# Performance work log

Measured on AMD Instinct MI355X. Metric: run time of the kernel, lower is better.

The kernel has to match this reference:

```python
import jax, jax.numpy as jnp
import numpy as np
from jax import lax

B, N, HID = 2, 2048, 2048
H, KVH, D = 16, 4, 128           # heads, kv heads, head_dim
GROUPS = H // KVH
FLA_WEIGHT = 0.01
NEG = -1e30


def setup_inputs() -> dict:
    key = jax.random.key(0)
    ks = jax.random.split(key, 5)
    s = 0.02
    return {
        "hidden_states": jax.random.normal(ks[0], (B, N, HID), jnp.float32),
        "Wq": jax.random.normal(ks[1], (HID, H * D), jnp.float32) * s,
        "Wk": jax.random.normal(ks[2], (HID, KVH * D), jnp.float32) * s,
        "Wv": jax.random.normal(ks[3], (HID, KVH * D), jnp.float32) * s,
        "Wo": jax.random.normal(ks[4], (H * D, HID), jnp.float32) * s,
    }


def _split_heads(x, h):
    b, n, _ = x.shape
    return x.reshape(b, n, h, -1).transpose(0, 2, 1, 3)  # b h n d


def _gla_attention(q, k, v, scale):
    # Gated linear attention: S_t = sigmoid(k_t) (.) S_{t-1} + k_t (x) v_t,
    # o_t = scale * q_t . S_t ; sequential recurrence over the seq dim.
    qs = jnp.moveaxis(q, 2, 0)  # n b h d
    ks = jnp.moveaxis(k, 2, 0)
    vs = jnp.moveaxis(v, 2, 0)

    def step(S, inp):
        qt, kt, vt = inp                                   # each (b,h,d)
        g = jax.nn.sigmoid(kt)                             # per-key-dim gate
        S = S * g[..., None] + kt[..., None] * vt[..., None, :]  # (b,h,d,dv)
        ot = scale * jnp.einsum('bhd,bhde->bhe', qt, S)
        return S, ot

    S0 = jnp.zeros(q.shape[:2] + (q.shape[-1], v.shape[-1]), q.dtype)
    _, o = lax.scan(step, S0, (qs, ks, vs))                # n b h dv
    return jnp.moveaxis(o, 0, 2)                           # b h n dv


def reference(hidden_states, Wq, Wk, Wv, Wo):
    scale = 1.0 / np.sqrt(D)
    q = _split_heads(hidden_states @ Wq, H)                # b h n d
    k = _split_heads(hidden_states @ Wk, KVH)
    v = _split_heads(hidden_states @ Wv, KVH)
    k = jnp.repeat(k, GROUPS, axis=1)                      # repeat_kv -> b H n d
    v = jnp.repeat(v, GROUPS, axis=1)

    # FLA branch
    fla = _gla_attention(q, k, v, scale)                   # b h n d
    fla = fla.transpose(0, 2, 1, 3).reshape(B, N, H * D)   # b n (h d)

    # Base causal softmax attention
    scores = jnp.einsum('bhnd,bhmd->bhnm', q, k) * scale
    causal = jnp.tril(jnp.ones((N, N), bool))
    scores = jnp.where(causal, scores, NEG)
    attn = jax.nn.softmax(scores, axis=-1)
    base = jnp.einsum('bhnm,bhmd->bhnd', attn, v)
    base = base.transpose(0, 2, 1, 3).reshape(B, N, H * D) @ Wo

    return base + FLA_WEIGHT * fla
```

## Files before the change

### kernel.cpp

```cpp
#include <hip/hip_runtime.h>
#include <hip/hip_bf16.h>
#include <cstdint>
#include <cstddef>


typedef __attribute__((ext_vector_type(4))) float f32x4;
typedef __attribute__((ext_vector_type(2))) float f32x2;
typedef __attribute__((ext_vector_type(8))) short s16x8;
typedef unsigned short u16;
typedef unsigned int u32;

__device__ __forceinline__ float bfu2f(u16 u) {
  union { unsigned int i; float f; } x; x.i = ((unsigned int)u) << 16; return x.f;
}
__device__ __forceinline__ u16 f2bfu(float f) {
  union { float f; unsigned int i; } x; x.f = f;
  unsigned int r = x.i + 0x7fffu + ((x.i >> 16) & 1u);
  return (u16)(r >> 16);
}
__device__ __forceinline__ void bf8_to_f(s16x8 v, float* o) {
  union { s16x8 v; u16 u[8]; } x; x.v = v;
#pragma unroll
  for (int j = 0; j < 8; j++) o[j] = bfu2f(x.u[j]);
}
__device__ __forceinline__ s16x8 pack_bf8(f32x4 lo, f32x4 hi) {
  union { s16x8 v; u16 u[8]; } x;
#pragma unroll
  for (int j = 0; j < 4; j++) { x.u[j] = f2bfu(lo[j]); x.u[4 + j] = f2bfu(hi[j]); }
  return x.v;
}
__device__ __forceinline__ void gload_lds16(const u16* g, u16* l) {
  __builtin_amdgcn_global_load_lds(
      (__attribute__((address_space(1))) void*)(g),
      (__attribute__((address_space(3))) void*)(l), 16, 0, 0);
}

__global__ __launch_bounds__(256) void f32_to_bf16(
    const float* __restrict__ src, u16* __restrict__ dst, int n8) {
  const int i = blockIdx.x * 256 + threadIdx.x;
  if (i < n8) {
    f32x4 a = *(const f32x4*)(src + (size_t)i * 8);
    f32x4 b = *(const f32x4*)(src + (size_t)i * 8 + 4);
    *(s16x8*)(dst + (size_t)i * 8) = pack_bf8(a, b);
  }
}

__global__ __launch_bounds__(256) void transpose_f32_bf16(
    const float* __restrict__ src, u16* __restrict__ dst, int R, int C) {
  __shared__ u16 tile[32][33];
  const int bx = blockIdx.x * 32, by = blockIdx.y * 32;
  const int tx = threadIdx.x & 31, ty = threadIdx.x >> 5;
#pragma unroll
  for (int i = 0; i < 32; i += 8)
    tile[ty + i][tx] = f2bfu(src[(size_t)(by + ty + i) * C + bx + tx]);
  __syncthreads();
#pragma unroll
  for (int i = 0; i < 32; i += 8)
    dst[(size_t)(bx + ty + i) * R + by + tx] = tile[tx][ty + i];
}

__global__ __launch_bounds__(256) void transpose_bf16(
    const u16* __restrict__ src, u16* __restrict__ dst, int R, int C) {
  __shared__ u16 tile[32][33];
  const int bx = blockIdx.x * 32, by = blockIdx.y * 32;
  const int tx = threadIdx.x & 31, ty = threadIdx.x >> 5;
#pragma unroll
  for (int i = 0; i < 32; i += 8)
    tile[ty + i][tx] = src[(size_t)(by + ty + i) * C + bx + tx];
  __syncthreads();
#pragma unroll
  for (int i = 0; i < 32; i += 8)
    dst[(size_t)(bx + ty + i) * R + by + tx] = tile[tx][ty + i];
}

__global__ __launch_bounds__(256) void gemm_qkv(
    const u16* __restrict__ A, const u16* __restrict__ WqT, const u16* __restrict__ WkT,
    const u16* __restrict__ WvT, u16* __restrict__ Qo, u16* __restrict__ Ko,
    u16* __restrict__ Vo) {
  __shared__ u16 Al[128 * 32];
  __shared__ u16 Bl[128 * 32];
  const int bx = blockIdx.x;
  const u16* Bt; u16* Cb; int n0, Nst;
  if (bx < 16)      { Bt = WqT; Cb = Qo; n0 = bx * 128;        Nst = 2048; }
  else if (bx < 20) { Bt = WkT; Cb = Ko; n0 = (bx - 16) * 128; Nst = 512; }
  else              { Bt = WvT; Cb = Vo; n0 = (bx - 20) * 128; Nst = 512; }
  const int K = 2048;
  const int m0 = blockIdx.y * 128;
  const int t = threadIdx.x, w = t >> 6, l = t & 63, lm = l & 15, lq = l >> 4;
  const int wr = w >> 1, wc = w & 1;
  const f32x4 z4 = {0.f, 0.f, 0.f, 0.f};
  f32x4 acc[4][4];
#pragma unroll
  for (int i = 0; i < 4; i++)
#pragma unroll
    for (int j = 0; j < 4; j++) acc[i][j] = z4;
  const int srow = l >> 2, scol = (l & 3) * 8;
  const u16* Ag = A + (size_t)(m0 + w * 32 + srow) * K + scol;
  const u16* Bg = Bt + (size_t)(n0 + w * 32 + srow) * K + scol;
  u16* Alw = &Al[(w * 32) * 32];
  u16* Blw = &Bl[(w * 32) * 32];
  for (int kk = 0; kk < K; kk += 32) {
    gload_lds16(Ag + kk, Alw);
    gload_lds16(Ag + (size_t)16 * K + kk, Alw + 16 * 32);
    gload_lds16(Bg + kk, Blw);
    gload_lds16(Bg + (size_t)16 * K + kk, Blw + 16 * 32);
    __syncthreads();
    s16x8 af[4], bfr[4];
#pragma unroll
    for (int sm = 0; sm < 4; sm++) af[sm] = *(const s16x8*)&Al[(wr * 64 + sm * 16 + lm) * 32 + lq * 8];
#pragma unroll
    for (int sn = 0; sn < 4; sn++) bfr[sn] = *(const s16x8*)&Bl[(wc * 64 + sn * 16 + lm) * 32 + lq * 8];
#pragma unroll
    for (int sm = 0; sm < 4; sm++)
#pragma unroll
      for (int sn = 0; sn < 4; sn++)
        acc[sm][sn] = __builtin_amdgcn_mfma_f32_16x16x32_bf16(af[sm], bfr[sn], acc[sm][sn], 0, 0, 0);
    __syncthreads();
  }
#pragma unroll
  for (int sm = 0; sm < 4; sm++)
#pragma unroll
    for (int sn = 0; sn < 4; sn++)
#pragma unroll
      for (int r = 0; r < 4; r++) {
        const int row = m0 + wr * 64 + sm * 16 + lq * 4 + r;
        const int col = n0 + wc * 64 + sn * 16 + lm;
        Cb[(size_t)row * Nst + col] = f2bfu(acc[sm][sn][r]);
      }
}

__global__ __launch_bounds__(512) void gemm_out2(
    const u16* __restrict__ A, const u16* __restrict__ Bt, float* __restrict__ Cf,
    const u16* __restrict__ addsrc) {
  __shared__ u16 Abuf[3 * 16384];
  __shared__ u16 Bbuf[3 * 8192];
  int f = blockIdx.y * 16 + blockIdx.x;
  f = (f & 7) * 32 + (f >> 3);
  const int by = f >> 4, bx = f & 15;
  const int m0 = by * 256, n0 = bx * 128;
  const int K = 2048, Nst = 2048;
  const int t = threadIdx.x, w = t >> 6, l = t & 63, lm = l & 15, lq = l >> 4;
  const int wr = w >> 1, wc = w & 1;
  const int tr = t >> 3, tc8 = (t & 7) * 8;
  const f32x4 z4 = {0.f, 0.f, 0.f, 0.f};
  f32x4 acc[4][4];
#pragma unroll
  for (int i = 0; i < 4; i++)
#pragma unroll
    for (int j = 0; j < 4; j++) acc[i][j] = z4;
  const u16* Ag = A + (size_t)m0 * K;
  const u16* Bg = Bt + (size_t)n0 * K;
  auto stage = [&](int kt, int bufi) {
#pragma unroll
    for (int i = 0; i < 4; i++) {
      const int row = i * 64 + tr;
      const int col = tc8 ^ ((row & 7) << 3);
      gload_lds16(Ag + (size_t)row * K + kt * 64 + col,
                  Abuf + bufi * 16384 + i * 4096 + w * 512);
    }
#pragma unroll
    for (int i = 0; i < 2; i++) {
      const int row = i * 64 + tr;
      const int col = tc8 ^ ((row & 7) << 3);
      gload_lds16(Bg + (size_t)row * K + kt * 64 + col,
                  Bbuf + bufi * 8192 + i * 4096 + w * 512);
    }
  };
  const int nt = K >> 6;
  stage(0, 0);
  stage(1, 1);
  int cur = 0;
#pragma unroll 1
  for (int kt = 0; kt < nt; kt++) {
    if (kt + 2 < nt) {
      int nb = cur + 2; if (nb >= 3) nb -= 3;
      stage(kt + 2, nb);
      asm volatile("s_waitcnt vmcnt(12)" ::: "memory");
    } else if (kt + 1 < nt) {
      asm volatile("s_waitcnt vmcnt(6)" ::: "memory");
    } else {
      asm volatile("s_waitcnt vmcnt(0)" ::: "memory");
    }
    __builtin_amdgcn_s_barrier();
    const u16* Ab = Abuf + cur * 16384;
    const u16* Bb = Bbuf + cur * 8192;
    s16x8 af[4][2], bff[4][2];
#pragma unroll
    for (int sm = 0; sm < 4; sm++) {
      const int row = wr * 64 + sm * 16 + lm;
#pragma unroll
      for (int kk = 0; kk < 2; kk++)
        af[sm][kk] = *(const s16x8*)&Ab[row * 64 +
            ((((kk << 6) | (lq << 4)) ^ ((row & 7) << 4)) >> 1)];
    }
#pragma unroll
    for (int sn = 0; sn < 4; sn++) {
      const int row = wc * 64 + sn * 16 + lm;
#pragma unroll
      for (int kk = 0; kk < 2; kk++)
        bff[sn][kk] = *(const s16x8*)&Bb[row * 64 +
            ((((kk << 6) | (lq << 4)) ^ ((row & 7) << 4)) >> 1)];
    }
#pragma unroll
    for (int kk = 0; kk < 2; kk++)
#pragma unroll
      for (int sm = 0; sm < 4; sm++)
#pragma unroll
        for (int sn = 0; sn < 4; sn++)
          acc[sm][sn] = __builtin_amdgcn_mfma_f32_16x16x32_bf16(
              af[sm][kk], bff[sn][kk], acc[sm][sn], 0, 0, 0);
    asm volatile("s_waitcnt lgkmcnt(0)" ::: "memory");
    __builtin_amdgcn_s_barrier();
    cur = (cur == 2) ? 0 : cur + 1;
  }
#pragma unroll
  for (int sm = 0; sm < 4; sm++)
#pragma unroll
    for (int sn = 0; sn < 4; sn++)
#pragma unroll
      for (int r = 0; r < 4; r++) {
        const int row = m0 + wr * 64 + sm * 16 + lq * 4 + r;
        const int col = n0 + wc * 64 + sn * 16 + lm;
        float v = acc[sm][sn][r] + 0.01f * bfu2f(addsrc[(size_t)row * Nst + col]);
        Cf[(size_t)row * Nst + col] = v;
      }
}

__global__ __launch_bounds__(512) void flash_attn_wave(
    const u16* __restrict__ Q, const u16* __restrict__ Kx,
    const u16* __restrict__ Vt, u16* __restrict__ AO) {
  __shared__ u16 Klds[2][64 * 128];
  __shared__ u16 Vlds[2][128 * 64];
  __shared__ u16 Pl[8][16][68];
  const int bid = blockIdx.x;
  const int set = bid & 7;
  const int b = set >> 2, kvh = set & 3;
  const int rest = bid >> 3;
  const int j0 = rest >> 1, hp = rest & 1;
  const int t = threadIdx.x, w = t >> 6, l = t & 63, lm = l & 15, lq = l >> 4;
  const int h = kvh * 4 + hp * 2 + (w & 1);
  const int cs = (w >> 1) & 1, mh = w >> 2;
  const float scale2 = 0.127517827f;
  const u16* Kbase = Kx + (size_t)(b * 2048) * 512 + kvh * 128;
  const u16* Vbase = Vt + (size_t)(b * 512 + kvh * 128) * 2048;
  const f32x4 z4 = {0.f, 0.f, 0.f, 0.f};

  auto stage = [&](int kt, int bufi) {
    const int key0 = kt * 64;
#pragma unroll
    for (int r = 0; r < 2; r++) {
      const int row = r * 32 + w * 4 + (l >> 4);
      const int scb = ((l & 15) * 16) ^ ((row & 7) << 4);
      gload_lds16(Kbase + (size_t)(key0 + row) * 512 + (scb >> 1),
                  &Klds[bufi][r * 4096 + w * 512]);
    }
#pragma unroll
    for (int r = 0; r < 2; r++) {
      const int row = r * 64 + w * 8 + (l >> 3);
      const int scb = ((l & 7) * 16) ^ ((row & 7) << 4);
      gload_lds16(Vbase + (size_t)row * 2048 + key0 + (scb >> 1),
                  &Vlds[bufi][r * 4096 + w * 512]);
    }
  };

#pragma unroll 1
  for (int ph = 0; ph < 2; ph++) {
    const int j = ph ? (31 - j0) : j0;
    const int c = 2 * j + cs;
    const int base = c * 32;
    int cur = 0;
    stage(0, 0);
    s16x8 qf[4];
#pragma unroll
    for (int kk = 0; kk < 4; kk++)
      qf[kk] = *(const s16x8*)(Q + ((size_t)(b * 2048 + base + mh * 16 + lm)) * 2048 +
                               h * 128 + kk * 32 + lq * 8);
    f32x4 oacc[8];
#pragma unroll
    for (int e = 0; e < 8; e++) oacc[e] = z4;
    float lsum[4] = {0.f, 0.f, 0.f, 0.f};
#pragma unroll 1
    for (int kt = 0; kt <= j; kt++) {
      const int key0 = kt * 64;
      if (kt < j) {
        stage(kt + 1, cur ^ 1);
        asm volatile("s_waitcnt vmcnt(4)" ::: "memory");
      } else {
        asm volatile("s_waitcnt vmcnt(0)" ::: "memory");
      }
      __builtin_amdgcn_s_barrier();
      const char* KB = (const char*)&Klds[cur][0];
      const char* VB = (const char*)&Vlds[cur][0];
      s16x8 kf[4][4];
#pragma unroll
      for (int nst = 0; nst < 4; nst++)
#pragma unroll
        for (int kk = 0; kk < 4; kk++) {
          const int row = nst * 16 + lm;
          const int cb = (kk * 64 + lq * 16) ^ ((row & 7) << 4);
          kf[nst][kk] = *(const s16x8*)(KB + row * 256 + cb);
        }
      f32x4 sacc[4];
#pragma unroll
      for (int i = 0; i < 4; i++) sacc[i] = z4;
#pragma unroll
      for (int nst = 0; nst < 4; nst++)
#pragma unroll
        for (int kk = 0; kk < 4; kk++)
          sacc[nst] = __builtin_amdgcn_mfma_f32_16x16x32_bf16(
              qf[kk], kf[nst][kk], sacc[nst], 0, 0, 0);
      const bool diag = (kt == j);
#pragma unroll
      for (int r = 0; r < 4; r++) {
        const int qrow = base + mh * 16 + lq * 4 + r;
#pragma unroll
        for (int nst = 0; nst < 4; nst++) {
          float pv = __builtin_amdgcn_exp2f(sacc[nst][r] * scale2);
          if (diag && (key0 + nst * 16 + lm > qrow)) pv = 0.f;
          lsum[r] += pv;
          Pl[w][lq * 4 + r][nst * 16 + lm] = f2bfu(pv);
        }
      }
      s16x8 vf[8][2];
#pragma unroll
      for (int et = 0; et < 8; et++)
#pragma unroll
        for (int kc = 0; kc < 2; kc++) {
          const int row = et * 16 + lm;
          const int cb = (kc * 64 + lq * 16) ^ ((row & 7) << 4);
          vf[et][kc] = *(const s16x8*)(VB + row * 128 + cb);
        }
      s16x8 pf[2];
#pragma unroll
      for (int kc = 0; kc < 2; kc++)
        pf[kc] = *(const s16x8*)&Pl[w][lm][kc * 32 + lq * 8];
#pragma unroll
      for (int et = 0; et < 8; et++)
#pragma unroll
        for (int kc = 0; kc < 2; kc++)
          oacc[et] = __builtin_amdgcn_mfma_f32_16x16x32_bf16(
              pf[kc], vf[et][kc], oacc[et], 0, 0, 0);
      asm volatile("s_waitcnt lgkmcnt(0)" ::: "memory");
      __builtin_amdgcn_s_barrier();
      cur ^= 1;
    }
#pragma unroll
    for (int r = 0; r < 4; r++) {
#pragma unroll
      for (int off = 1; off < 16; off <<= 1)
        lsum[r] += __shfl_xor(lsum[r], off, 64);
    }
#pragma unroll
    for (int r = 0; r < 4; r++) {
      const float inv = 1.f / lsum[r];
      const int row = base + mh * 16 + lq * 4 + r;
      u16* op = AO + ((size_t)(b * 2048 + row)) * 2048 + h * 128;
#pragma unroll
      for (int et = 0; et < 8; et++) op[et * 16 + lm] = f2bfu(oacc[et][r] * inv);
    }
  }
}

__global__ __launch_bounds__(256) void fla_contrib32(
    const u16* __restrict__ Kx, const u16* __restrict__ Vt,
    u16* __restrict__ Gg, u16* __restrict__ Ktg, u16* __restrict__ MT,
    float* __restrict__ Lam) {
  __shared__ float gl[32][132];
  __shared__ float kl[32][132];
  __shared__ float ktl[32][132];
  __shared__ u16 khT[128][40];
  const int c = blockIdx.x, kvh = blockIdx.y, b = blockIdx.z;
  const int bk = b * 4 + kvh;
  const int t = threadIdx.x;
  const size_t cb = (size_t)bk * 64 + c;
  {
    const int r = t >> 3, c0 = (t & 7) * 16;
    const u16* kp = Kx + ((size_t)(b * 2048 + c * 32 + r)) * 512 + kvh * 128 + c0;
#pragma unroll
    for (int i = 0; i < 2; i++) {
      float kv[8];
      bf8_to_f(*(const s16x8*)(kp + i * 8), kv);
#pragma unroll
      for (int j = 0; j < 8; j++) {
        kl[r][c0 + i * 8 + j] = kv[j];
        gl[r][c0 + i * 8 + j] = 1.f / (1.f + __expf(-kv[j]));
      }
    }
  }
  __syncthreads();
  if (t < 128) {
    float G = 1.f;
#pragma unroll
    for (int s = 0; s < 32; s++) {
      G *= gl[s][t];
      gl[s][t] = G;
      ktl[s][t] = kl[s][t] / G;
    }
    Lam[cb * 128 + t] = G;
    const float lam = G;
#pragma unroll
    for (int s = 0; s < 32; s++) khT[t][s] = f2bfu(ktl[s][t] * lam);
  }
  __syncthreads();
  {
    const int r = t >> 3, c0 = (t & 7) * 16;
    u16* gp = Gg + cb * 4096 + r * 128 + c0;
    u16* kp = Ktg + cb * 4096 + r * 128 + c0;
#pragma unroll
    for (int i = 0; i < 2; i++) {
      f32x4 a = *(f32x4*)&gl[r][c0 + i * 8];
      f32x4 b2 = *(f32x4*)&gl[r][c0 + i * 8 + 4];
      *(s16x8*)(gp + i * 8) = pack_bf8(a, b2);
      a = *(f32x4*)&ktl[r][c0 + i * 8];
      b2 = *(f32x4*)&ktl[r][c0 + i * 8 + 4];
      *(s16x8*)(kp + i * 8) = pack_bf8(a, b2);
    }
  }
  const int w = t >> 6, l = t & 63, lm = l & 15, lq = l >> 4;
  const f32x4 z4 = {0.f, 0.f, 0.f, 0.f};
  f32x4 macc[2][8];
#pragma unroll
  for (int ei = 0; ei < 2; ei++)
#pragma unroll
    for (int dt = 0; dt < 8; dt++) macc[ei][dt] = z4;
  s16x8 vtf[2];
#pragma unroll
  for (int ei = 0; ei < 2; ei++) {
    const int et = w * 2 + ei;
    vtf[ei] = *(const s16x8*)(Vt + ((size_t)(b * 512 + kvh * 128 + et * 16 + lm)) * 2048 +
                              c * 32 + lq * 8);
  }
#pragma unroll
  for (int dt = 0; dt < 8; dt++) {
    s16x8 kf = *(const s16x8*)&khT[dt * 16 + lm][lq * 8];
#pragma unroll
    for (int ei = 0; ei < 2; ei++)
      macc[ei][dt] = __builtin_amdgcn_mfma_f32_16x16x32_bf16(vtf[ei], kf, macc[ei][dt], 0, 0, 0);
  }
  u16* mp = MT + cb * 16384;
#pragma unroll
  for (int ei = 0; ei < 2; ei++)
#pragma unroll
    for (int dt = 0; dt < 8; dt++)
#pragma unroll
      for (int r = 0; r < 4; r++)
        mp[(size_t)((w * 2 + ei) * 16 + lq * 4 + r) * 128 + dt * 16 + lm] =
            f2bfu(macc[ei][dt][r]);
}

__global__ __launch_bounds__(256) void fla_prefix32(
    const u16* __restrict__ MT, const float* __restrict__ Lam, u16* __restrict__ SwsT) {
  const int eg = blockIdx.x, bk = blockIdx.y;
  const int t = threadIdx.x;
  const int e = eg * 4 + (t >> 6), d0 = (t & 63) * 2;
  const size_t cb0 = (size_t)bk * 64;
  const u16* mp = MT + cb0 * 16384 + e * 128 + d0;
  const float* lp = Lam + cb0 * 128 + d0;
  u16* sp = SwsT + cb0 * 16384 + e * 128 + d0;
  float s0 = 0.f, s1 = 0.f;
  u32 ma = *(const u32*)mp;
  u32 mb = *(const u32*)(mp + 16384);
  f32x2 la = *(const f32x2*)lp;
  f32x2 lb = *(const f32x2*)(lp + 128);
#pragma unroll 1
  for (int c = 0; c < 64; c += 2) {
    u32 na = 0, nb = 0;
    f32x2 nla = {0.f, 0.f}, nlb = {0.f, 0.f};
    if (c + 2 < 64) {
      na = *(const u32*)(mp + (size_t)(c + 2) * 16384);
      nla = *(const f32x2*)(lp + (size_t)(c + 2) * 128);
      nb = *(const u32*)(mp + (size_t)(c + 3) * 16384);
      nlb = *(const f32x2*)(lp + (size_t)(c + 3) * 128);
    }
    *(u32*)(sp + (size_t)c * 16384) = (u32)f2bfu(s0) | ((u32)f2bfu(s1) << 16);
    s0 = s0 * la[0] + bfu2f((u16)(ma & 0xffffu));
    s1 = s1 * la[1] + bfu2f((u16)(ma >> 16));
    *(u32*)(sp + (size_t)(c + 1) * 16384) = (u32)f2bfu(s0) | ((u32)f2bfu(s1) << 16);
    s0 = s0 * lb[0] + bfu2f((u16)(mb & 0xffffu));
    s1 = s1 * lb[1] + bfu2f((u16)(mb >> 16));
    ma = na; mb = nb; la = nla; lb = nlb;
  }
}

__global__ __launch_bounds__(256) void fla_output_mfma(
    const u16* __restrict__ Q, const u16* __restrict__ Gg, const u16* __restrict__ Ktg,
    const u16* __restrict__ SwsT, const u16* __restrict__ Vt, u16* __restrict__ Fla) {
  __shared__ u16 Pl[4][2][16][40];
  const int c = blockIdx.x, h = blockIdx.y, b = blockIdx.z;
  const int kvh = h >> 2, bk = b * 4 + kvh;
  const int t = threadIdx.x, w = t >> 6, l = t & 63, lm = l & 15, lq = l >> 4;
  const float scale = 0.0883883476483184f;
  const size_t cb = (size_t)bk * 64 + c;
  const f32x4 z4 = {0.f, 0.f, 0.f, 0.f};
  s16x8 qgf[2][4];
#pragma unroll
  for (int m = 0; m < 2; m++)
#pragma unroll
    for (int kk = 0; kk < 4; kk++) {
      float qv[8], gv[8];
      bf8_to_f(*(const s16x8*)(Q + ((size_t)(b * 2048 + c * 32 + m * 16 + lm)) * 2048 +
                               h * 128 + kk * 32 + lq * 8), qv);
      bf8_to_f(*(const s16x8*)(Gg + cb * 4096 + (m * 16 + lm) * 128 + kk * 32 + lq * 8), gv);
      f32x4 a, b2;
#pragma unroll
      for (int j = 0; j < 4; j++) { a[j] = qv[j] * gv[j]; b2[j] = qv[4 + j] * gv[4 + j]; }
      qgf[m][kk] = pack_bf8(a, b2);
    }
  f32x4 sacc[2][2];
#pragma unroll
  for (int m = 0; m < 2; m++)
#pragma unroll
    for (int st = 0; st < 2; st++) sacc[m][st] = z4;
#pragma unroll
  for (int st = 0; st < 2; st++)
#pragma unroll
    for (int kk = 0; kk < 4; kk++) {
      s16x8 ktf = *(const s16x8*)(Ktg + cb * 4096 + (st * 16 + lm) * 128 + kk * 32 + lq * 8);
#pragma unroll
      for (int m = 0; m < 2; m++)
        sacc[m][st] = __builtin_amdgcn_mfma_f32_16x16x32_bf16(qgf[m][kk], ktf, sacc[m][st], 0, 0, 0);
    }
#pragma unroll
  for (int m = 0; m < 2; m++)
#pragma unroll
    for (int st = 0; st < 2; st++)
#pragma unroll
      for (int r = 0; r < 4; r++) {
        const int trow = m * 16 + lq * 4 + r;
        const int scol = st * 16 + lm;
        Pl[w][m][lq * 4 + r][st * 16 + lm] = f2bfu(scol <= trow ? sacc[m][st][r] : 0.f);
      }
  s16x8 pf[2];
#pragma unroll
  for (int m = 0; m < 2; m++) pf[m] = *(const s16x8*)&Pl[w][m][lm][lq * 8];
  f32x4 oacc[2][2];
#pragma unroll
  for (int m = 0; m < 2; m++)
#pragma unroll
    for (int ei = 0; ei < 2; ei++) oacc[m][ei] = z4;
#pragma unroll
  for (int ei = 0; ei < 2; ei++) {
    const int et = w * 2 + ei;
    s16x8 vtf = *(const s16x8*)(Vt + ((size_t)(b * 512 + kvh * 128 + et * 16 + lm)) * 2048 +
                                c * 32 + lq * 8);
#pragma unroll
    for (int m = 0; m < 2; m++)
      oacc[m][ei] = __builtin_amdgcn_mfma_f32_16x16x32_bf16(pf[m], vtf, oacc[m][ei], 0, 0, 0);
#pragma unroll
    for (int kk = 0; kk < 4; kk++) {
      s16x8 s0f = *(const s16x8*)(SwsT + cb * 16384 + (et * 16 + lm) * 128 + kk * 32 + lq * 8);
#pragma unroll
      for (int m = 0; m < 2; m++)
        oacc[m][ei] = __builtin_amdgcn_mfma_f32_16x16x32_bf16(qgf[m][kk], s0f, oacc[m][ei], 0, 0, 0);
    }
  }
#pragma unroll
  for (int m = 0; m < 2; m++)
#pragma unroll
    for (int ei = 0; ei < 2; ei++)
#pragma unroll
      for (int r = 0; r < 4; r++)
        Fla[((size_t)(b * 2048 + c * 32 + m * 16 + lq * 4 + r)) * 2048 + h * 128 +
            (w * 2 + ei) * 16 + lm] = f2bfu(scale * oacc[m][ei][r]);
}

extern "C" void kernel_launch(void* const* d_in, const int* in_sizes, int n_in,
                              void* d_out, int out_size, void* d_ws, size_t ws_size,
                              hipStream_t stream) {
  const float* X  = (const float*)d_in[0];
  const float* Wq = (const float*)d_in[1];
  const float* Wk = (const float*)d_in[2];
  const float* Wv = (const float*)d_in[3];
  const float* Wo = (const float*)d_in[4];
  float* out = (float*)d_out;

  char* ws = (char*)d_ws;
  size_t off = 0;
  auto alloc = [&](size_t bytes) { void* p = ws + off; off += (bytes + 255) & ~(size_t)255; return p; };
  u16* WoT = (u16*)alloc(2048ull * 2048 * 2);
  u16* Qb  = (u16*)alloc(4096ull * 2048 * 2);
  u16* Kb  = (u16*)alloc(4096ull * 512 * 2);
  u16* Vb  = (u16*)alloc(4096ull * 512 * 2);
  u16* Vtb = (u16*)alloc(2ull * 512 * 2048 * 2);
  u16* Fla = (u16*)alloc(4096ull * 2048 * 2);
  u16* SH16 = (u16*)alloc(4096ull * 2048 * 2);
  u16* Xb = SH16;
  u16* MT = SH16;
  u16* AO = SH16;
  char* BIG = (char*)alloc(26ull * 1024 * 1024);
  u16* WqT = (u16*)BIG;
  u16* WkT = (u16*)(BIG + 8ull * 1024 * 1024);
  u16* WvT = (u16*)(BIG + 10ull * 1024 * 1024);
  u16* Gg   = (u16*)BIG;
  u16* Ktg  = (u16*)(BIG + 4194304ull);
  u16* SwsT = (u16*)(BIG + 8388608ull);
  float* Lam = (float*)(BIG + 8388608ull + 16777216ull);
  (void)ws_size; (void)in_sizes; (void)n_in; (void)out_size;

  dim3 blk(256);
  f32_to_bf16<<<dim3(4096), blk, 0, stream>>>(X, Xb, 4096 * 2048 / 8);
  transpose_f32_bf16<<<dim3(64, 64), blk, 0, stream>>>(Wq, WqT, 2048, 2048);
  transpose_f32_bf16<<<dim3(16, 64), blk, 0, stream>>>(Wk, WkT, 2048, 512);
  transpose_f32_bf16<<<dim3(16, 64), blk, 0, stream>>>(Wv, WvT, 2048, 512);
  transpose_f32_bf16<<<dim3(64, 64), blk, 0, stream>>>(Wo, WoT, 2048, 2048);

  gemm_qkv<<<dim3(24, 32), blk, 0, stream>>>(Xb, WqT, WkT, WvT, Qb, Kb, Vb);

  transpose_bf16<<<dim3(16, 64), blk, 0, stream>>>(Vb, Vtb, 2048, 512);
  transpose_bf16<<<dim3(16, 64), blk, 0, stream>>>(Vb + 2048ull * 512, Vtb + 512ull * 2048, 2048, 512);

  fla_contrib32<<<dim3(64, 4, 2), blk, 0, stream>>>(Kb, Vtb, Gg, Ktg, MT, Lam);
  fla_prefix32<<<dim3(32, 8), blk, 0, stream>>>(MT, Lam, SwsT);
  fla_output_mfma<<<dim3(64, 16, 2), blk, 0, stream>>>(Qb, Gg, Ktg, SwsT, Vtb, Fla);

  flash_attn_wave<<<dim3(256), dim3(512), 0, stream>>>(Qb, Kb, Vtb, AO);

  gemm_out2<<<dim3(16, 16), dim3(512), 0, stream>>>(AO, WoT, out, Fla);
}
```

Before: 353.7 us.

## Split flash-attention blocks per query chunk, batch transposes, add MFMA priority and packed bf16 converts

Merges the four weight transposes into one launch and the two V transposes into one 3D launch, cutting launch overhead. The flash attention kernel no longer pairs a light and a heavy causal query chunk per block. It launches 512 blocks, each handling one chunk, which gives more parallelism but loses the load balancing the pairing provided. It also adds s_setprio around the MFMA sections, uses v_cvt_pk_bf16_f32 for packing P, and removes padding on the P LDS buffer, which may introduce bank conflicts.

```diff
diff --git a/kernel.cpp b/kernel.cpp
--- a/kernel.cpp
+++ b/kernel.cpp
@@ -45,10 +45,18 @@
   }
 }
 
-__global__ __launch_bounds__(256) void transpose_f32_bf16(
-    const float* __restrict__ src, u16* __restrict__ dst, int R, int C) {
+__global__ __launch_bounds__(256) void transpose_w4(
+    const float* __restrict__ Wq, const float* __restrict__ Wk,
+    const float* __restrict__ Wv, const float* __restrict__ Wo,
+    u16* __restrict__ WqT, u16* __restrict__ WkT,
+    u16* __restrict__ WvT, u16* __restrict__ WoT) {
   __shared__ u16 tile[32][33];
-  const int bx = blockIdx.x * 32, by = blockIdx.y * 32;
+  const int bid = blockIdx.x;
+  const float* src; u16* dst; int R, C, bx, by;
+  if (bid < 4096)      { src = Wq; dst = WqT; R = 2048; C = 2048; bx = (bid & 63) * 32; by = (bid >> 6) * 32; }
+  else if (bid < 5120) { const int v = bid - 4096; src = Wk; dst = WkT; R = 2048; C = 512;  bx = (v & 15) * 32; by = (v >> 4) * 32; }
+  else if (bid < 6144) { const int v = bid - 5120; src = Wv; dst = WvT; R = 2048; C = 512;  bx = (v & 15) * 32; by = (v >> 4) * 32; }
+  else                 { const int v = bid - 6144; src = Wo; dst = WoT; R = 2048; C = 2048; bx = (v & 63) * 32; by = (v >> 6) * 32; }
   const int tx = threadIdx.x & 31, ty = threadIdx.x >> 5;
 #pragma unroll
   for (int i = 0; i < 32; i += 8)
@@ -59,9 +67,12 @@
     dst[(size_t)(bx + ty + i) * R + by + tx] = tile[tx][ty + i];
 }
 
-__global__ __launch_bounds__(256) void transpose_bf16(
-    const u16* __restrict__ src, u16* __restrict__ dst, int R, int C) {
+__global__ __launch_bounds__(256) void transpose_bf16v(
+    const u16* __restrict__ src0, u16* __restrict__ dst0) {
   __shared__ u16 tile[32][33];
+  const int R = 2048, C = 512;
+  const u16* src = src0 + (size_t)blockIdx.z * 2048 * 512;
+  u16* dst = dst0 + (size_t)blockIdx.z * 512 * 2048;
   const int bx = blockIdx.x * 32, by = blockIdx.y * 32;
   const int tx = threadIdx.x & 31, ty = threadIdx.x >> 5;
 #pragma unroll
@@ -231,12 +242,12 @@
     const u16* __restrict__ Vt, u16* __restrict__ AO) {
   __shared__ u16 Klds[2][64 * 128];
   __shared__ u16 Vlds[2][128 * 64];
-  __shared__ u16 Pl[8][16][68];
+  __shared__ u16 Pl[8][16][64];
   const int bid = blockIdx.x;
   const int set = bid & 7;
   const int b = set >> 2, kvh = set & 3;
   const int rest = bid >> 3;
-  const int j0 = rest >> 1, hp = rest & 1;
+  const int j = rest >> 1, hp = rest & 1;
   const int t = threadIdx.x, w = t >> 6, l = t & 63, lm = l & 15, lq = l >> 4;
   const int h = kvh * 4 + hp * 2 + (w & 1);
   const int cs = (w >> 1) & 1, mh = w >> 2;
@@ -263,101 +274,116 @@
     }
   };
 
+  const int c = 2 * j + cs;
+  const int base = c * 32;
+  int cur = 0;
+  stage(0, 0);
+  s16x8 qf[4];
+#pragma unroll
+  for (int kk = 0; kk < 4; kk++)
+    qf[kk] = *(const s16x8*)(Q + ((size_t)(b * 2048 + base + mh * 16 + lm)) * 2048 +
+                             h * 128 + kk * 32 + lq * 8);
+  f32x4 oacc[8];
+#pragma unroll
+  for (int e = 0; e < 8; e++) oacc[e] = z4;
+  float lsum[4] = {0.f, 0.f, 0.f, 0.f};
 #pragma unroll 1
-  for (int ph = 0; ph < 2; ph++) {
-    const int j = ph ? (31 - j0) : j0;
-    const int c = 2 * j + cs;
-    const int base = c * 32;
-    int cur = 0;
-    stage(0, 0);
-    s16x8 qf[4];
-#pragma unroll
-    for (int kk = 0; kk < 4; kk++)
-      qf[kk] = *(const s16x8*)(Q + ((size_t)(b * 2048 + base + mh * 16 + lm)) * 2048 +
-                               h * 128 + kk * 32 + lq * 8);
-    f32x4 oacc[8];
-#pragma unroll
-    for (int e = 0; e < 8; e++) oacc[e] = z4;
-    float lsum[4] = {0.f, 0.f, 0.f, 0.f};
-#pragma unroll 1
-    for (int kt = 0; kt <= j; kt++) {
-      const int key0 = kt * 64;
-      if (kt < j) {
-        stage(kt + 1, cur ^ 1);
-        asm volatile("s_waitcnt vmcnt(4)" ::: "memory");
-      } else {
-        asm volatile("s_waitcnt vmcnt(0)" ::: "memory");
+  for (int kt = 0; kt <= j; kt++) {
+    const int key0 = kt * 64;
+    if (kt < j) {
+      stage(kt + 1, cur ^ 1);
+      asm volatile("s_waitcnt vmcnt(4)" ::: "memory");
+    } else {
+      asm volatile("s_waitcnt vmcnt(0)" ::: "memory");
+    }
+    __builtin_amdgcn_s_barrier();
+    const char* KB = (const char*)&Klds[cur][0];
+    const char* VB = (const char*)&Vlds[cur][0];
+    s16x8 kf[4][4];
+#pragma unroll
+    for (int nst = 0; nst < 4; nst++)
+#pragma unroll
+      for (int kk = 0; kk < 4; kk++) {
+        const int row = nst * 16 + lm;
+        const int cb = (kk * 64 + lq * 16) ^ ((row & 7) << 4);
+        kf[nst][kk] = *(const s16x8*)(KB + row * 256 + cb);
       }
-      __builtin_amdgcn_s_barrier();
-      const char* KB = (const char*)&Klds[cur][0];
-      const char* VB = (const char*)&Vlds[cur][0];
-      s16x8 kf[4][4];
+    f32x4 sacc[4];
+#pragma unroll
+    for (int i = 0; i < 4; i++) sacc[i] = z4;
+    __builtin_amdgcn_s_setprio(1);
+#pragma unroll
+    for (int nst = 0; nst < 4; nst++)
+#pragma unroll
+      for (int kk = 0; kk < 4; kk++)
+        sacc[nst] = __builtin_amdgcn_mfma_f32_16x16x32_bf16(
+            qf[kk], kf[nst][kk], sacc[nst], 0, 0, 0);
+    __builtin_amdgcn_s_setprio(0);
+    float pv[4][4];
+#pragma unroll
+    for (int r = 0; r < 4; r++)
 #pragma unroll
       for (int nst = 0; nst < 4; nst++)
-#pragma unroll
-        for (int kk = 0; kk < 4; kk++) {
-          const int row = nst * 16 + lm;
-          const int cb = (kk * 64 + lq * 16) ^ ((row & 7) << 4);
-          kf[nst][kk] = *(const s16x8*)(KB + row * 256 + cb);
-        }
-      f32x4 sacc[4];
-#pragma unroll
-      for (int i = 0; i < 4; i++) sacc[i] = z4;
-#pragma unroll
-      for (int nst = 0; nst < 4; nst++)
-#pragma unroll
-        for (int kk = 0; kk < 4; kk++)
-          sacc[nst] = __builtin_amdgcn_mfma_f32_16x16x32_bf16(
-              qf[kk], kf[nst][kk], sacc[nst], 0, 0, 0);
-      const bool diag = (kt == j);
+        pv[r][nst] = __builtin_amdgcn_exp2f(sacc[nst][r] * scale2);
+    if (kt == j) {
 #pragma unroll
       for (int r = 0; r < 4; r++) {
         const int qrow = base + mh * 16 + lq * 4 + r;
 #pragma unroll
-        for (int nst = 0; nst < 4; nst++) {
-          float pv = __builtin_amdgcn_exp2f(sacc[nst][r] * scale2);
-          if (diag && (key0 + nst * 16 + lm > qrow)) pv = 0.f;
-          lsum[r] += pv;
-          Pl[w][lq * 4 + r][nst * 16 + lm] = f2bfu(pv);
-        }
+        for (int nst = 0; nst < 4; nst++)
+          if (key0 + nst * 16 + lm > qrow) pv[r][nst] = 0.f;
       }
-      s16x8 vf[8][2];
-#pragma unroll
-      for (int et = 0; et < 8; et++)
-#pragma unroll
-        for (int kc = 0; kc < 2; kc++) {
-          const int row = et * 16 + lm;
-          const int cb = (kc * 64 + lq * 16) ^ ((row & 7) << 4);
-          vf[et][kc] = *(const s16x8*)(VB + row * 128 + cb);
-        }
-      s16x8 pf[2];
+    }
+#pragma unroll
+    for (int r = 0; r < 4; r++) {
+      lsum[r] += (pv[r][0] + pv[r][1]) + (pv[r][2] + pv[r][3]);
+      u32 p01, p23;
+      asm("v_cvt_pk_bf16_f32 %0, %1, %2" : "=v"(p01) : "v"(pv[r][0]), "v"(pv[r][1]));
+      asm("v_cvt_pk_bf16_f32 %0, %1, %2" : "=v"(p23) : "v"(pv[r][2]), "v"(pv[r][3]));
+      u16* prow = &Pl[w][lq * 4 + r][lm];
+      prow[0]  = (u16)p01;
+      prow[16] = (u16)(p01 >> 16);
+      prow[32] = (u16)p23;
+      prow[48] = (u16)(p23 >> 16);
+    }
+    s16x8 vf[8][2];
+#pragma unroll
+    for (int et = 0; et < 8; et++)
+#pragma unroll
+      for (int kc = 0; kc < 2; kc++) {
+        const int row = et * 16 + lm;
+        const int cb = (kc * 64 + lq * 16) ^ ((row & 7) << 4);
+        vf[et][kc] = *(const s16x8*)(VB + row * 128 + cb);
+      }
+    s16x8 pf[2];
+#pragma unroll
+    for (int kc = 0; kc < 2; kc++)
+      pf[kc] = *(const s16x8*)&Pl[w][lm][kc * 32 + lq * 8];
+    __builtin_amdgcn_s_setprio(1);
+#pragma unroll
+    for (int et = 0; et < 8; et++)
 #pragma unroll
       for (int kc = 0; kc < 2; kc++)
-        pf[kc] = *(const s16x8*)&Pl[w][lm][kc * 32 + lq * 8];
-#pragma unroll
-      for (int et = 0; et < 8; et++)
-#pragma unroll
-        for (int kc = 0; kc < 2; kc++)
-          oacc[et] = __builtin_amdgcn_mfma_f32_16x16x32_bf16(
-              pf[kc], vf[et][kc], oacc[et], 0, 0, 0);
-      asm volatile("s_waitcnt lgkmcnt(0)" ::: "memory");
-      __builtin_amdgcn_s_barrier();
-      cur ^= 1;
-    }
-#pragma unroll
-    for (int r = 0; r < 4; r++) {
-#pragma unroll
-      for (int off = 1; off < 16; off <<= 1)
-        lsum[r] += __shfl_xor(lsum[r], off, 64);
-    }
-#pragma unroll
-    for (int r = 0; r < 4; r++) {
-      const float inv = 1.f / lsum[r];
-      const int row = base + mh * 16 + lq * 4 + r;
-      u16* op = AO + ((size_t)(b * 2048 + row)) * 2048 + h * 128;
-#pragma unroll
-      for (int et = 0; et < 8; et++) op[et * 16 + lm] = f2bfu(oacc[et][r] * inv);
-    }
+        oacc[et] = __builtin_amdgcn_mfma_f32_16x16x32_bf16(
+            pf[kc], vf[et][kc], oacc[et], 0, 0, 0);
+    __builtin_amdgcn_s_setprio(0);
+    asm volatile("s_waitcnt lgkmcnt(0)" ::: "memory");
+    __builtin_amdgcn_s_barrier();
+    cur ^= 1;
+  }
+#pragma unroll
+  for (int r = 0; r < 4; r++) {
+#pragma unroll
+    for (int off = 1; off < 16; off <<= 1)
+      lsum[r] += __shfl_xor(lsum[r], off, 64);
+  }
+#pragma unroll
+  for (int r = 0; r < 4; r++) {
+    const float inv = 1.f / lsum[r];
+    const int row = base + mh * 16 + lq * 4 + r;
+    u16* op = AO + ((size_t)(b * 2048 + row)) * 2048 + h * 128;
+#pragma unroll
+    for (int et = 0; et < 8; et++) op[et * 16 + lm] = f2bfu(oacc[et][r] * inv);
   }
 }
 
@@ -599,21 +625,17 @@
 
   dim3 blk(256);
   f32_to_bf16<<<dim3(4096), blk, 0, stream>>>(X, Xb, 4096 * 2048 / 8);
-  transpose_f32_bf16<<<dim3(64, 64), blk, 0, stream>>>(Wq, WqT, 2048, 2048);
-  transpose_f32_bf16<<<dim3(16, 64), blk, 0, stream>>>(Wk, WkT, 2048, 512);
-  transpose_f32_bf16<<<dim3(16, 64), blk, 0, stream>>>(Wv, WvT, 2048, 512);
-  transpose_f32_bf16<<<dim3(64, 64), blk, 0, stream>>>(Wo, WoT, 2048, 2048);
+  transpose_w4<<<dim3(10240), blk, 0, stream>>>(Wq, Wk, Wv, Wo, WqT, WkT, WvT, WoT);
 
   gemm_qkv<<<dim3(24, 32), blk, 0, stream>>>(Xb, WqT, WkT, WvT, Qb, Kb, Vb);
 
-  transpose_bf16<<<dim3(16, 64), blk, 0, stream>>>(Vb, Vtb, 2048, 512);
-  transpose_bf16<<<dim3(16, 64), blk, 0, stream>>>(Vb + 2048ull * 512, Vtb + 512ull * 2048, 2048, 512);
+  transpose_bf16v<<<dim3(16, 64, 2), blk, 0, stream>>>(Vb, Vtb);
 
   fla_contrib32<<<dim3(64, 4, 2), blk, 0, stream>>>(Kb, Vtb, Gg, Ktg, MT, Lam);
   fla_prefix32<<<dim3(32, 8), blk, 0, stream>>>(MT, Lam, SwsT);
   fla_output_mfma<<<dim3(64, 16, 2), blk, 0, stream>>>(Qb, Gg, Ktg, SwsT, Vtb, Fla);
 
-  flash_attn_wave<<<dim3(256), dim3(512), 0, stream>>>(Qb, Kb, Vtb, AO);
+  flash_attn_wave<<<dim3(512), dim3(512), 0, stream>>>(Qb, Kb, Vtb, AO);
 
   gemm_out2<<<dim3(16, 16), dim3(512), 0, stream>>>(AO, WoT, out, Fla);
 }
```

New measurement: 374.1 us. 1.06x slower.
